# Kernel tuning notes

Measured on AMD Instinct MI355X. Metric: run time of the kernel, lower is better.

The kernel has to match this reference:

```python
import jax, jax.numpy as jnp
import numpy as np

L = 5  # history window (init kwarg)

def _mlp(x, W1, b1, W2, b2, W3, b3):
    h = jax.nn.relu(x @ W1 + b1)
    h = jax.nn.relu(h @ W2 + b2)
    return h @ W3 + b3

def setup_inputs() -> dict:
    key = jax.random.key(0)
    ks = jax.random.split(key, 12)
    N, T1, S, D, H, E = 2000, 11, 5, 64, 256, 100000
    IN = 2 * D + 2 * L * S + 3 + 1 + 1  # 183
    return {
        "features": jax.random.normal(ks[0], (N, D), jnp.float32),
        "states": jax.random.uniform(ks[1], (N, T1, S), jnp.float32),
        "distances": jax.random.uniform(ks[2], (N, N), jnp.float32),
        "W1": jax.random.normal(ks[3], (IN, H), jnp.float32) * 0.05,
        "b1": jnp.zeros((H,), jnp.float32),
        "W2": jax.random.normal(ks[4], (H, H), jnp.float32) * 0.05,
        "b2": jnp.zeros((H,), jnp.float32),
        "W3": jax.random.normal(ks[5], (H, 3), jnp.float32) * 0.05,
        "b3": jnp.zeros((3,), jnp.float32),
        "pairs_i": jax.random.randint(ks[6], (E,), 0, N, jnp.int32),
        "pairs_j": jax.random.randint(ks[7], (E,), 0, N, jnp.int32),
        "max_timestep": 10,
    }

def reference(features, states, distances, W1, b1, W2, b2, W3, b3, pairs_i, pairs_j, max_timestep):
    T = int(max_timestep)  # static
    N, T1, S = states.shape
    E = pairs_i.shape[0]
    # --- state histories: hist[t, n] = states[n, max(0,t-L+1)..t] zero-padded, flattened to L*S
    pad = jnp.pad(states, ((0, 0), (L - 1, 0), (0, 0)))  # [N, T1+L-1, S]
    idx = jnp.arange(T + 1)[:, None] + jnp.arange(L)[None, :]  # [T+1, L]
    hist = pad[:, idx, :]  # [N, T+1, L, S]
    hist = jnp.transpose(hist, (1, 0, 2, 3)).reshape(T + 1, N, L * S)
    hist = jax.lax.stop_gradient(hist)  # original .detach()

    fi = features[pairs_i]              # [E, D]
    fj = features[pairs_j]              # [E, D]
    dist = distances[pairs_i, pairs_j][:, None]  # [E, 1]
    eye3 = jnp.eye(3, dtype=features.dtype)

    # --- t = 0: is_initial=1, dummy prev type = onehot(0); same conditional for all k_prev
    x0 = jnp.concatenate([
        fi, fj, hist[0, pairs_i], hist[0, pairs_j],
        jnp.broadcast_to(eye3[0], (E, 3)), dist, jnp.ones_like(dist)
    ], axis=-1)
    p0 = jax.nn.softmax(_mlp(x0, W1, b1, W2, b2, W3, b3), axis=-1)  # [E, 3]
    cond0 = jnp.broadcast_to(p0[:, None, :], (E, 3, 3))              # [E, 3, 3]
    m0 = p0

    # --- t >= 1: one NN call on 3 stacked prev-type branches, then forward-algo recursion
    hp_i = hist[1:, pairs_i]  # [T, E, L*S]
    hp_j = hist[1:, pairs_j]
    prev3 = jnp.broadcast_to(eye3[:, None, :], (3, E, 3))
    tail = jnp.concatenate([dist, jnp.zeros_like(dist)], axis=-1)  # [E, 2] (dist, is_initial=0)

    def step(m_prev, xs):
        hi, hj = xs
        base = jnp.concatenate([fi, fj, hi, hj], axis=-1)  # [E, 2D+2LS]
        x = jnp.concatenate([
            jnp.broadcast_to(base[None], (3, E, base.shape[-1])),
            prev3,
            jnp.broadcast_to(tail[None], (3, E, 2)),
        ], axis=-1)  # [3, E, IN]
        probs = jax.nn.softmax(_mlp(x, W1, b1, W2, b2, W3, b3), axis=-1)  # [3, E, 3]
        cond = jnp.transpose(probs, (1, 0, 2))  # [E, k_prev, k_next]
        m = jnp.einsum('ek,ekn->en', m_prev, cond)
        return m, (cond, m)

    _, (conds, margs) = jax.lax.scan(step, m0, (hp_i, hp_j))
    conditionals = jnp.concatenate([cond0[None], conds], axis=0)  # [T+1, E, 3, 3]
    marginals = jnp.concatenate([m0[None], margs], axis=0)        # [T+1, E, 3]
    return conditionals, marginals
```

## Files before the change

kernel.cpp:

```cpp
#include <hip/hip_runtime.h>
#include <hip/hip_bf16.h>
#include <math.h>

#define D_F   64
#define IN_F  183
#define KS1   6
#define KS2   8
#define HID   256
#define HPITCH 264
#define BM    64
#define BLK   512

typedef unsigned short u16;
typedef __attribute__((ext_vector_type(8))) short bf16x8;
typedef __attribute__((ext_vector_type(4))) float f32x4;

__device__ __forceinline__ u16 f2bf(float v) {
    __hip_bfloat16 h = __float2bfloat16(v);
    u16 u; __builtin_memcpy(&u, &h, 2); return u;
}

__global__ void pack_w_kernel(const float* __restrict__ W, u16* __restrict__ Wp,
                              int K, int KSs)
{
    int g = blockIdx.x * 256 + threadIdx.x;
    int total = 16 * KSs * 64;
    if (g >= total) return;
    int lane = g & 63;
    int ks   = (g >> 6) % KSs;
    int mt   = (g >> 6) / KSs;
    int col  = mt * 16 + (lane & 15);
    int kb   = ks * 32 + 8 * (lane >> 4);
    u16 out[8];
    #pragma unroll
    for (int j = 0; j < 8; ++j) {
        int k = kb + j;
        out[j] = f2bf((k < K) ? W[(size_t)k * HID + col] : 0.0f);
    }
    *(bf16x8*)(Wp + (size_t)g * 8) = *(const bf16x8*)out;
}

__global__ __launch_bounds__(BLK)
void mfp_mlp_mfma(const float* __restrict__ features,
                  const float* __restrict__ states,
                  const float* __restrict__ distances,
                  const float* __restrict__ W1,
                  const u16* __restrict__ W1p, const float* __restrict__ b1,
                  const u16* __restrict__ W2p, const float* __restrict__ b2,
                  const float* __restrict__ W3, const float* __restrict__ b3,
                  const int* __restrict__ pairs_i, const int* __restrict__ pairs_j,
                  float* __restrict__ cond,
                  int N, int T1s, int E, int T)
{
    extern __shared__ char smem[];
    u16* hsA = (u16*)smem;
    __shared__ int   s_pi[BM], s_pj[BM], s_e[BM], s_val[BM];
    __shared__ float s_dist[BM];
    __shared__ float s_w3[HID][4];
    __shared__ float s_plog[4][BM][3];

    const int tid = threadIdx.x;
    const int t   = blockIdx.y;
    const int nk  = (t == 0) ? 1 : 3;

    if (tid < BM) {
        int pe = blockIdx.x * BM + tid;
        int valid = (pe < E) ? 1 : 0;
        int e = valid ? pe : 0;
        int pi = pairs_i[e], pj = pairs_j[e];
        s_e[tid] = e; s_val[tid] = valid; s_pi[tid] = pi; s_pj[tid] = pj;
        s_dist[tid] = distances[(long long)pi * N + pj];
    }
    for (int idx = tid; idx < HID * 4; idx += BLK) {
        int h = idx >> 2, n = idx & 3;
        s_w3[h][n] = (n < 3) ? W3[h * 3 + n] : 0.0f;
    }
    __syncthreads();

    u16* xs = hsA;
    for (int idx = tid; idx < BM * 32; idx += BLK) {
        int m = idx >> 5;
        int q = idx & 31;
        int src = (q < 16) ? s_pi[m] : s_pj[m];
        int c4  = (q & 15) * 4;
        float4 f = *(const float4*)&features[(size_t)src * D_F + c4];
        int c = ((q < 16) ? 0 : 64) + c4;
        ushort4 o;
        o.x = f2bf(f.x); o.y = f2bf(f.y); o.z = f2bf(f.z); o.w = f2bf(f.w);
        *(ushort4*)(xs + m * HPITCH + c) = o;
    }
    for (int idx = tid; idx < BM * 64; idx += BLK) {
        int m = idx >> 6;
        int c = 128 + (idx & 63);
        float v;
        if (c < 178) {
            int cc = c - 128;
            int row = (cc < 25) ? s_pi[m] : s_pj[m];
            int c2  = (cc < 25) ? cc : (cc - 25);
            int l = c2 / 5;
            int s = c2 - l * 5;
            int tau = t - 4 + l;
            v = (tau >= 0) ? states[((size_t)row * T1s + tau) * 5 + s] : 0.0f;
        } else if (c == 181) {
            v = s_dist[m];
        } else if (c == 182) {
            v = (t == 0) ? 1.0f : 0.0f;
        } else {
            v = 0.0f;
        }
        xs[m * HPITCH + c] = f2bf(v);
    }
    __syncthreads();

    const int lane = tid & 63;
    const int w    = tid >> 6;
    const int a    = w & 3;
    const int b    = w >> 2;
    const int lr   = lane & 15;
    const int lg   = lane >> 4;

    f32x4 acc1[4][2];
    #pragma unroll
    for (int i = 0; i < 4; ++i)
        #pragma unroll
        for (int j = 0; j < 2; ++j)
            acc1[i][j] = (f32x4){0.f, 0.f, 0.f, 0.f};

    for (int ks = 0; ks < KS1; ++ks) {
        bf16x8 wfr[4];
        #pragma unroll
        for (int mtl = 0; mtl < 4; ++mtl)
            wfr[mtl] = *(const bf16x8*)(W1p + (((size_t)(4 * a + mtl) * KS1 + ks) * 64 + lane) * 8);
        bf16x8 xfr[2];
        #pragma unroll
        for (int ntl = 0; ntl < 2; ++ntl)
            xfr[ntl] = *(const bf16x8*)(xs + (32 * b + 16 * ntl + lr) * HPITCH + ks * 32 + 8 * lg);
        #pragma unroll
        for (int mtl = 0; mtl < 4; ++mtl)
            #pragma unroll
            for (int ntl = 0; ntl < 2; ++ntl)
                acc1[mtl][ntl] = __builtin_amdgcn_mfma_f32_16x16x32_bf16(wfr[mtl], xfr[ntl], acc1[mtl][ntl], 0, 0, 0);
    }

    for (int k = 0; k < nk; ++k) {
        __syncthreads();

        #pragma unroll
        for (int mtl = 0; mtl < 4; ++mtl) {
            int h0 = 16 * (4 * a + mtl) + 4 * lg;
            f32x4 b1q = *(const f32x4*)&b1[h0];
            f32x4 ohq = *(const f32x4*)&W1[(size_t)(178 + k) * HID + h0];
            #pragma unroll
            for (int ntl = 0; ntl < 2; ++ntl) {
                ushort4 p;
                p.x = f2bf(fmaxf(acc1[mtl][ntl][0] + b1q[0] + ohq[0], 0.0f));
                p.y = f2bf(fmaxf(acc1[mtl][ntl][1] + b1q[1] + ohq[1], 0.0f));
                p.z = f2bf(fmaxf(acc1[mtl][ntl][2] + b1q[2] + ohq[2], 0.0f));
                p.w = f2bf(fmaxf(acc1[mtl][ntl][3] + b1q[3] + ohq[3], 0.0f));
                *(ushort4*)(hsA + (32 * b + 16 * ntl + lr) * HPITCH + h0) = p;
            }
        }
        __syncthreads();

        f32x4 acc2[4][2];
        #pragma unroll
        for (int i = 0; i < 4; ++i)
            #pragma unroll
            for (int j = 0; j < 2; ++j)
                acc2[i][j] = (f32x4){0.f, 0.f, 0.f, 0.f};

        for (int ks = 0; ks < KS2; ++ks) {
            bf16x8 wfr[4];
            #pragma unroll
            for (int mtl = 0; mtl < 4; ++mtl)
                wfr[mtl] = *(const bf16x8*)(W2p + (((size_t)(4 * a + mtl) * KS2 + ks) * 64 + lane) * 8);
            bf16x8 hfr[2];
            #pragma unroll
            for (int ntl = 0; ntl < 2; ++ntl)
                hfr[ntl] = *(const bf16x8*)(hsA + (32 * b + 16 * ntl + lr) * HPITCH + ks * 32 + 8 * lg);
            #pragma unroll
            for (int mtl = 0; mtl < 4; ++mtl)
                #pragma unroll
                for (int ntl = 0; ntl < 2; ++ntl)
                    acc2[mtl][ntl] = __builtin_amdgcn_mfma_f32_16x16x32_bf16(wfr[mtl], hfr[ntl], acc2[mtl][ntl], 0, 0, 0);
        }

        float part[2][3];
        part[0][0] = 0.f; part[0][1] = 0.f; part[0][2] = 0.f;
        part[1][0] = 0.f; part[1][1] = 0.f; part[1][2] = 0.f;

        #pragma unroll
        for (int mtl = 0; mtl < 4; ++mtl) {
            int h0 = 16 * (4 * a + mtl) + 4 * lg;
            f32x4 b2q = *(const f32x4*)&b2[h0];
            f32x4 w3r[4];
            #pragma unroll
            for (int r = 0; r < 4; ++r)
                w3r[r] = *(const f32x4*)&s_w3[h0 + r][0];
            #pragma unroll
            for (int ntl = 0; ntl < 2; ++ntl)
                #pragma unroll
                for (int r = 0; r < 4; ++r) {
                    float h2 = fmaxf(acc2[mtl][ntl][r] + b2q[r], 0.0f);
                    part[ntl][0] = fmaf(h2, w3r[r][0], part[ntl][0]);
                    part[ntl][1] = fmaf(h2, w3r[r][1], part[ntl][1]);
                    part[ntl][2] = fmaf(h2, w3r[r][2], part[ntl][2]);
                }
        }
        #pragma unroll
        for (int ntl = 0; ntl < 2; ++ntl)
            #pragma unroll
            for (int n = 0; n < 3; ++n) {
                part[ntl][n] += __shfl_xor(part[ntl][n], 16, 64);
                part[ntl][n] += __shfl_xor(part[ntl][n], 32, 64);
            }
        if (lg == 0) {
            #pragma unroll
            for (int ntl = 0; ntl < 2; ++ntl) {
                int m = 32 * b + 16 * ntl + lr;
                s_plog[a][m][0] = part[ntl][0];
                s_plog[a][m][1] = part[ntl][1];
                s_plog[a][m][2] = part[ntl][2];
            }
        }
        __syncthreads();

        if (tid < BM && s_val[tid]) {
            int m = tid;
            float l0 = s_plog[0][m][0] + s_plog[1][m][0] + s_plog[2][m][0] + s_plog[3][m][0] + b3[0];
            float l1 = s_plog[0][m][1] + s_plog[1][m][1] + s_plog[2][m][1] + s_plog[3][m][1] + b3[1];
            float l2 = s_plog[0][m][2] + s_plog[1][m][2] + s_plog[2][m][2] + s_plog[3][m][2] + b3[2];
            float mx = fmaxf(l0, fmaxf(l1, l2));
            float e0 = expf(l0 - mx), e1 = expf(l1 - mx), e2 = expf(l2 - mx);
            float inv = 1.0f / (e0 + e1 + e2);
            float p0 = e0 * inv, p1 = e1 * inv, p2 = e2 * inv;
            size_t base = ((size_t)t * E + s_e[m]) * 9;
            if (t == 0) {
                #pragma unroll
                for (int kb = 0; kb < 3; ++kb) {
                    cond[base + kb * 3 + 0] = p0;
                    cond[base + kb * 3 + 1] = p1;
                    cond[base + kb * 3 + 2] = p2;
                }
            } else {
                cond[base + k * 3 + 0] = p0;
                cond[base + k * 3 + 1] = p1;
                cond[base + k * 3 + 2] = p2;
            }
        }
    }
}

__global__ __launch_bounds__(256)
void mfp_marg_kernel(const float* __restrict__ cond,
                     float* __restrict__ marg,
                     int E, int T)
{
    int e = blockIdx.x * 256 + threadIdx.x;
    if (e >= E) return;
    const float* c0 = &cond[(size_t)e * 9];
    float m0 = c0[0], m1 = c0[1], m2 = c0[2];
    marg[(size_t)e * 3 + 0] = m0;
    marg[(size_t)e * 3 + 1] = m1;
    marg[(size_t)e * 3 + 2] = m2;
    for (int t = 1; t <= T; ++t) {
        const float* c9 = &cond[((size_t)t * E + e) * 9];
        float n0 = m0 * c9[0] + m1 * c9[3] + m2 * c9[6];
        float n1 = m0 * c9[1] + m1 * c9[4] + m2 * c9[7];
        float n2 = m0 * c9[2] + m1 * c9[5] + m2 * c9[8];
        m0 = n0; m1 = n1; m2 = n2;
        float* mo = &marg[((size_t)t * E + e) * 3];
        mo[0] = m0; mo[1] = m1; mo[2] = m2;
    }
}

extern "C" void kernel_launch(void* const* d_in, const int* in_sizes, int n_in,
                              void* d_out, int out_size, void* d_ws, size_t ws_size,
                              hipStream_t stream) {
    const float* features  = (const float*)d_in[0];
    const float* states    = (const float*)d_in[1];
    const float* distances = (const float*)d_in[2];
    const float* W1 = (const float*)d_in[3];
    const float* b1 = (const float*)d_in[4];
    const float* W2 = (const float*)d_in[5];
    const float* b2 = (const float*)d_in[6];
    const float* W3 = (const float*)d_in[7];
    const float* b3 = (const float*)d_in[8];
    const int* pairs_i = (const int*)d_in[9];
    const int* pairs_j = (const int*)d_in[10];

    const int N   = in_sizes[0] / D_F;
    const int T1s = in_sizes[1] / (N * 5);
    const int E   = in_sizes[9];
    const int T   = out_size / (12 * E) - 1;

    float* cond = (float*)d_out;
    float* marg = (float*)d_out + (size_t)(T + 1) * E * 9;

    u16* W1p = (u16*)d_ws;
    u16* W2p = W1p + 16 * KS1 * 64 * 8;

    {
        int g1 = 16 * KS1 * 64;
        int g2 = 16 * KS2 * 64;
        pack_w_kernel<<<(g1 + 255) / 256, 256, 0, stream>>>(W1, W1p, IN_F, KS1);
        pack_w_kernel<<<(g2 + 255) / 256, 256, 0, stream>>>(W2, W2p, HID, KS2);
    }

    dim3 grid((E + BM - 1) / BM, T + 1);
    const size_t lds_bytes = (size_t)BM * HPITCH * sizeof(u16);

    mfp_mlp_mfma<<<grid, BLK, lds_bytes, stream>>>(
        features, states, distances, W1, W1p, b1, W2p, b2, W3, b3,
        pairs_i, pairs_j, cond, N, T1s, E, T);

    mfp_marg_kernel<<<(E + 255) / 256, 256, 0, stream>>>(cond, marg, E, T);
}
```

Measured before the change: 1.034 ms.

## Double the pair tile, run the final layer on MFMA, double-buffer hidden activations

```diff
diff --git a/kernel.cpp b/kernel.cpp
--- a/kernel.cpp
+++ b/kernel.cpp
@@ -8,8 +8,8 @@
 #define KS2   8
 #define HID   256
 #define HPITCH 264
-#define BM    64
-#define BLK   512
+#define BM    128
+#define BLK   1024
 
 typedef unsigned short u16;
 typedef __attribute__((ext_vector_type(8))) short bf16x8;
@@ -40,6 +40,21 @@
     *(bf16x8*)(Wp + (size_t)g * 8) = *(const bf16x8*)out;
 }
 
+__global__ void pack_w3_kernel(const float* __restrict__ W3, u16* __restrict__ W3p)
+{
+    int g = blockIdx.x * 256 + threadIdx.x;
+    if (g >= KS2 * 64) return;
+    int lane = g & 63;
+    int ks   = g >> 6;
+    int n    = lane & 15;
+    int kb   = ks * 32 + 8 * (lane >> 4);
+    u16 out[8];
+    #pragma unroll
+    for (int j = 0; j < 8; ++j)
+        out[j] = f2bf((n < 3) ? W3[(size_t)(kb + j) * 3 + n] : 0.0f);
+    *(bf16x8*)(W3p + (size_t)g * 8) = *(const bf16x8*)out;
+}
+
 __global__ __launch_bounds__(BLK)
 void mfp_mlp_mfma(const float* __restrict__ features,
                   const float* __restrict__ states,
@@ -47,17 +62,16 @@
                   const float* __restrict__ W1,
                   const u16* __restrict__ W1p, const float* __restrict__ b1,
                   const u16* __restrict__ W2p, const float* __restrict__ b2,
-                  const float* __restrict__ W3, const float* __restrict__ b3,
+                  const u16* __restrict__ W3p, const float* __restrict__ b3,
                   const int* __restrict__ pairs_i, const int* __restrict__ pairs_j,
                   float* __restrict__ cond,
                   int N, int T1s, int E, int T)
 {
     extern __shared__ char smem[];
     u16* hsA = (u16*)smem;
+    u16* hsB = hsA + BM * HPITCH;
     __shared__ int   s_pi[BM], s_pj[BM], s_e[BM], s_val[BM];
     __shared__ float s_dist[BM];
-    __shared__ float s_w3[HID][4];
-    __shared__ float s_plog[4][BM][3];
 
     const int tid = threadIdx.x;
     const int t   = blockIdx.y;
@@ -70,10 +84,6 @@
         int pi = pairs_i[e], pj = pairs_j[e];
         s_e[tid] = e; s_val[tid] = valid; s_pi[tid] = pi; s_pj[tid] = pj;
         s_dist[tid] = distances[(long long)pi * N + pj];
-    }
-    for (int idx = tid; idx < HID * 4; idx += BLK) {
-        int h = idx >> 2, n = idx & 3;
-        s_w3[h][n] = (n < 3) ? W3[h * 3 + n] : 0.0f;
     }
     __syncthreads();
 
@@ -142,9 +152,11 @@
                 acc1[mtl][ntl] = __builtin_amdgcn_mfma_f32_16x16x32_bf16(wfr[mtl], xfr[ntl], acc1[mtl][ntl], 0, 0, 0);
     }
 
+    const float b30 = b3[0], b31 = b3[1], b32 = b3[2];
+
+    __syncthreads();
+
     for (int k = 0; k < nk; ++k) {
-        __syncthreads();
-
         #pragma unroll
         for (int mtl = 0; mtl < 4; ++mtl) {
             int h0 = 16 * (4 * a + mtl) + 4 * lg;
@@ -185,69 +197,54 @@
                     acc2[mtl][ntl] = __builtin_amdgcn_mfma_f32_16x16x32_bf16(wfr[mtl], hfr[ntl], acc2[mtl][ntl], 0, 0, 0);
         }
 
-        float part[2][3];
-        part[0][0] = 0.f; part[0][1] = 0.f; part[0][2] = 0.f;
-        part[1][0] = 0.f; part[1][1] = 0.f; part[1][2] = 0.f;
-
         #pragma unroll
         for (int mtl = 0; mtl < 4; ++mtl) {
             int h0 = 16 * (4 * a + mtl) + 4 * lg;
             f32x4 b2q = *(const f32x4*)&b2[h0];
-            f32x4 w3r[4];
-            #pragma unroll
-            for (int r = 0; r < 4; ++r)
-                w3r[r] = *(const f32x4*)&s_w3[h0 + r][0];
-            #pragma unroll
-            for (int ntl = 0; ntl < 2; ++ntl)
-                #pragma unroll
-                for (int r = 0; r < 4; ++r) {
-                    float h2 = fmaxf(acc2[mtl][ntl][r] + b2q[r], 0.0f);
-                    part[ntl][0] = fmaf(h2, w3r[r][0], part[ntl][0]);
-                    part[ntl][1] = fmaf(h2, w3r[r][1], part[ntl][1]);
-                    part[ntl][2] = fmaf(h2, w3r[r][2], part[ntl][2]);
+            #pragma unroll
+            for (int ntl = 0; ntl < 2; ++ntl) {
+                ushort4 p;
+                p.x = f2bf(fmaxf(acc2[mtl][ntl][0] + b2q[0], 0.0f));
+                p.y = f2bf(fmaxf(acc2[mtl][ntl][1] + b2q[1], 0.0f));
+                p.z = f2bf(fmaxf(acc2[mtl][ntl][2] + b2q[2], 0.0f));
+                p.w = f2bf(fmaxf(acc2[mtl][ntl][3] + b2q[3], 0.0f));
+                *(ushort4*)(hsB + (32 * b + 16 * ntl + lr) * HPITCH + h0) = p;
+            }
+        }
+        __syncthreads();
+
+        if (w < 8) {
+            f32x4 acc3 = (f32x4){0.f, 0.f, 0.f, 0.f};
+            for (int ks = 0; ks < KS2; ++ks) {
+                bf16x8 hfr = *(const bf16x8*)(hsB + (w * 16 + lr) * HPITCH + ks * 32 + 8 * lg);
+                bf16x8 wfr = *(const bf16x8*)(W3p + ((size_t)(ks * 64 + lane)) * 8);
+                acc3 = __builtin_amdgcn_mfma_f32_16x16x32_bf16(wfr, hfr, acc3, 0, 0, 0);
+            }
+            int m = 16 * w + lr;
+            if (lg == 0 && s_val[m]) {
+                float l0 = acc3[0] + b30;
+                float l1 = acc3[1] + b31;
+                float l2 = acc3[2] + b32;
+                float mx = fmaxf(l0, fmaxf(l1, l2));
+                float e0 = expf(l0 - mx), e1 = expf(l1 - mx), e2 = expf(l2 - mx);
+                float inv = 1.0f / (e0 + e1 + e2);
+                float p0 = e0 * inv, p1 = e1 * inv, p2 = e2 * inv;
+                size_t base = ((size_t)t * E + s_e[m]) * 9;
+                if (t == 0) {
+                    #pragma unroll
+                    for (int kb = 0; kb < 3; ++kb) {
+                        cond[base + kb * 3 + 0] = p0;
+                        cond[base + kb * 3 + 1] = p1;
+                        cond[base + kb * 3 + 2] = p2;
+                    }
+                } else {
+                    cond[base + k * 3 + 0] = p0;
+                    cond[base + k * 3 + 1] = p1;
+                    cond[base + k * 3 + 2] = p2;
                 }
-        }
-        #pragma unroll
-        for (int ntl = 0; ntl < 2; ++ntl)
-            #pragma unroll
-            for (int n = 0; n < 3; ++n) {
-                part[ntl][n] += __shfl_xor(part[ntl][n], 16, 64);
-                part[ntl][n] += __shfl_xor(part[ntl][n], 32, 64);
             }
-        if (lg == 0) {
-            #pragma unroll
-            for (int ntl = 0; ntl < 2; ++ntl) {
-                int m = 32 * b + 16 * ntl + lr;
-                s_plog[a][m][0] = part[ntl][0];
-                s_plog[a][m][1] = part[ntl][1];
-                s_plog[a][m][2] = part[ntl][2];
-            }
         }
         __syncthreads();
-
-        if (tid < BM && s_val[tid]) {
-            int m = tid;
-            float l0 = s_plog[0][m][0] + s_plog[1][m][0] + s_plog[2][m][0] + s_plog[3][m][0] + b3[0];
-            float l1 = s_plog[0][m][1] + s_plog[1][m][1] + s_plog[2][m][1] + s_plog[3][m][1] + b3[1];
-            float l2 = s_plog[0][m][2] + s_plog[1][m][2] + s_plog[2][m][2] + s_plog[3][m][2] + b3[2];
-            float mx = fmaxf(l0, fmaxf(l1, l2));
-            float e0 = expf(l0 - mx), e1 = expf(l1 - mx), e2 = expf(l2 - mx);
-            float inv = 1.0f / (e0 + e1 + e2);
-            float p0 = e0 * inv, p1 = e1 * inv, p2 = e2 * inv;
-            size_t base = ((size_t)t * E + s_e[m]) * 9;
-            if (t == 0) {
-                #pragma unroll
-                for (int kb = 0; kb < 3; ++kb) {
-                    cond[base + kb * 3 + 0] = p0;
-                    cond[base + kb * 3 + 1] = p1;
-                    cond[base + kb * 3 + 2] = p2;
-                }
-            } else {
-                cond[base + k * 3 + 0] = p0;
-                cond[base + k * 3 + 1] = p1;
-                cond[base + k * 3 + 2] = p2;
-            }
-        }
     }
 }
 
@@ -299,19 +296,22 @@
 
     u16* W1p = (u16*)d_ws;
     u16* W2p = W1p + 16 * KS1 * 64 * 8;
+    u16* W3p = W2p + 16 * KS2 * 64 * 8;
 
     {
         int g1 = 16 * KS1 * 64;
         int g2 = 16 * KS2 * 64;
+        int g3 = KS2 * 64;
         pack_w_kernel<<<(g1 + 255) / 256, 256, 0, stream>>>(W1, W1p, IN_F, KS1);
         pack_w_kernel<<<(g2 + 255) / 256, 256, 0, stream>>>(W2, W2p, HID, KS2);
+        pack_w3_kernel<<<(g3 + 255) / 256, 256, 0, stream>>>(W3, W3p);
     }
 
     dim3 grid((E + BM - 1) / BM, T + 1);
-    const size_t lds_bytes = (size_t)BM * HPITCH * sizeof(u16);
+    const size_t lds_bytes = (size_t)2 * BM * HPITCH * sizeof(u16);
 
     mfp_mlp_mfma<<<grid, BLK, lds_bytes, stream>>>(
-        features, states, distances, W1, W1p, b1, W2p, b2, W3, b3,
+        features, states, distances, W1, W1p, b1, W2p, b2, W3p, b3,
         pairs_i, pairs_j, cond, N, T1s, E, T);
 
     mfp_marg_kernel<<<(E + 255) / 256, 256, 0, stream>>>(cond, marg, E, T);
```

Result: slower. 3.172 ms (+206.7%).
